# Kernel tuning notes

Hardware: AMD Instinct MI355X
Metric: run time of the kernel (lower is better)

## Reference

```python
import jax, jax.numpy as jnp
import numpy as np

B, N, D = 32, 2048, 1024


def setup_inputs() -> dict:
    key = jax.random.key(0)
    k1, k2, k3, k4, k5, k6 = jax.random.split(key, 6)
    encoded = jax.random.normal(k1, (B, N, D), dtype=jnp.float32)
    decoder_state = jax.random.normal(k2, (B, D), dtype=jnp.float32)
    mask = jax.random.randint(k3, (B, N), 0, 2, dtype=jnp.int32)
    scale = 1.0 / np.sqrt(D)
    W1 = jax.random.normal(k4, (D, D), dtype=jnp.float32) * scale  # applied as x @ W1
    W2 = jax.random.normal(k5, (D, D), dtype=jnp.float32) * scale
    vt = jax.random.normal(k6, (D,), dtype=jnp.float32) * scale
    return {"encoded": encoded, "decoder_state": decoder_state, "mask": mask,
            "W1": W1, "W2": W2, "vt": vt}


def reference(encoded, decoder_state, mask, W1, W2, vt):
    temperature = 1.0
    # process_encoded: W1(encoded)  [B, N, D]
    enc = jnp.einsum('bnd,de->bne', encoded, W1)
    # W2(decoder_state)  [B, D] -> broadcast-add over N
    dec = decoder_state @ W2
    # vt(tanh(.)).squeeze(2)  -> logits [B, N]
    u = jnp.einsum('bnd,d->bn', jnp.tanh(enc + dec[:, None, :]), vt)
    # masked log-softmax with temperature over dim=1
    logits = u / temperature + jnp.log(mask.astype(u.dtype) + 1e-45)
    return jax.nn.log_softmax(logits, axis=1)
```

## Files before the change

### kernel.cpp

```cpp
#include <hip/hip_runtime.h>

typedef _Float16 half8 __attribute__((ext_vector_type(8)));
typedef __fp16   pk2   __attribute__((ext_vector_type(2)));
typedef float    f32x4 __attribute__((ext_vector_type(4)));

#define GLOBAL_AS __attribute__((address_space(1)))
#define LDS_AS    __attribute__((address_space(3)))

static constexpr int Bb = 32;
static constexpr int Nn = 2048;
static constexpr int Dd = 1024;
static constexpr int M  = Bb * Nn;

__global__ void prep_w1(const float* __restrict__ W1, _Float16* __restrict__ W1TT) {
    int g = blockIdx.x * 256 + threadIdx.x;
    int tile = g >> 9;
    int u = g & 511;
    int et = tile >> 5, kt = tile & 31;
    int q = u >> 7, e = u & 127;
    int d0 = kt * 32 + q * 8;
    int col = et * 128 + e;
    half8 h;
#pragma unroll
    for (int j = 0; j < 8; ++j)
        h[j] = (_Float16)W1[(size_t)(d0 + j) * Dd + col];
    *(half8*)(W1TT + (size_t)g * 8) = h;
}

__global__ void prep_enc(const float* __restrict__ A, _Float16* __restrict__ A_p) {
    int g = blockIdx.x * 256 + threadIdx.x;
    int tile = g >> 9;
    int v = g & 511;
    int row = v >> 2, kc = v & 3;
    const float* src = A + ((size_t)(tile >> 5) * 128 + row) * Dd
                         + (tile & 31) * 32 + kc * 8;
    f32x4 f0 = *(const f32x4*)src;
    f32x4 f1 = *(const f32x4*)(src + 4);
    half8 h;
    pk2 t;
    t = __builtin_amdgcn_cvt_pkrtz(f0.x, f0.y); h[0] = t[0]; h[1] = t[1];
    t = __builtin_amdgcn_cvt_pkrtz(f0.z, f0.w); h[2] = t[0]; h[3] = t[1];
    t = __builtin_amdgcn_cvt_pkrtz(f1.x, f1.y); h[4] = t[0]; h[5] = t[1];
    t = __builtin_amdgcn_cvt_pkrtz(f1.z, f1.w); h[6] = t[0]; h[7] = t[1];
    *(half8*)(A_p + (size_t)g * 8) = h;
}

__global__ void dec_kernel(const float* __restrict__ ds, const float* __restrict__ W2,
                           float* __restrict__ dec) {
    __shared__ float part[4][64];
    int b = blockIdx.x, ech = blockIdx.y;
    int tid = threadIdx.x;
    int e = ech * 64 + (tid & 63);
    int dc = tid >> 6;
    float acc = 0.f;
#pragma unroll 4
    for (int d = dc * 256; d < dc * 256 + 256; ++d)
        acc += ds[b * Dd + d] * W2[(size_t)d * Dd + e];
    part[dc][tid & 63] = acc;
    __syncthreads();
    if (tid < 64)
        dec[b * Dd + e] = part[0][tid] + part[1][tid] + part[2][tid] + part[3][tid];
}

__global__ __launch_bounds__(256) void gemm_fused_h(
    const _Float16* __restrict__ A_p,
    const _Float16* __restrict__ W1TT,
    const float* __restrict__ dec,
    const float* __restrict__ vt,
    float* __restrict__ u_part)
{
    __shared__ _Float16 As[4096];
    __shared__ _Float16 Bs[4096];
    __shared__ float usum[2][128];

    const int g = blockIdx.x;
    const int et = (g >> 3) & 7;
    const int mtile = (g & 7) + ((g >> 6) << 3);
    const int tid = threadIdx.x;
    const int lane = tid & 63, wid = tid >> 6;
    const int wm = wid & 1, we = wid >> 1;
    const int q = lane >> 4, l15 = lane & 15;

    f32x4 acc[4][4] = {};

    const _Float16* abase = A_p + (size_t)mtile * 32 * 4096
                            + ((size_t)(wid * 2) * 64 + lane) * 8;
    const _Float16* bbase = W1TT + (size_t)et * 32 * 4096
                            + ((size_t)(wid * 2) * 64 + lane) * 8;
    _Float16* adst0 = &As[(wid * 2 + 0) * 64 * 8];
    _Float16* adst1 = &As[(wid * 2 + 1) * 64 * 8];
    _Float16* bdst0 = &Bs[(wid * 2 + 0) * 64 * 8];
    _Float16* bdst1 = &Bs[(wid * 2 + 1) * 64 * 8];

#pragma unroll 1
    for (int kt = 0; kt < 32; ++kt) {
        const _Float16* ak = abase + (size_t)kt * 4096;
        const _Float16* bk = bbase + (size_t)kt * 4096;
        __builtin_amdgcn_global_load_lds((const GLOBAL_AS void*)ak,
                                         (LDS_AS void*)adst0, 16, 0, 0);
        __builtin_amdgcn_global_load_lds((const GLOBAL_AS void*)(ak + 64 * 8),
                                         (LDS_AS void*)adst1, 16, 0, 0);
        __builtin_amdgcn_global_load_lds((const GLOBAL_AS void*)bk,
                                         (LDS_AS void*)bdst0, 16, 0, 0);
        __builtin_amdgcn_global_load_lds((const GLOBAL_AS void*)(bk + 64 * 8),
                                         (LDS_AS void*)bdst1, 16, 0, 0);
        __syncthreads();

        half8 af[4], bf[4];
#pragma unroll
        for (int mt = 0; mt < 4; ++mt)
            af[mt] = *(const half8*)&As[(wm * 64 + mt * 16 + l15) * 32 + q * 8];
#pragma unroll
        for (int nt = 0; nt < 4; ++nt)
            bf[nt] = *(const half8*)&Bs[(q * 128 + we * 64 + nt * 16 + l15) * 8];
#pragma unroll
        for (int mt = 0; mt < 4; ++mt)
#pragma unroll
            for (int nt = 0; nt < 4; ++nt)
                acc[mt][nt] = __builtin_amdgcn_mfma_f32_16x16x32_f16(
                    af[mt], bf[nt], acc[mt][nt], 0, 0, 0);
        __syncthreads();
    }

    const int b = mtile >> 4;
    float vtv[4], dcv[4];
#pragma unroll
    for (int nt = 0; nt < 4; ++nt) {
        int e = et * 128 + we * 64 + nt * 16 + l15;
        vtv[nt] = vt[e];
        dcv[nt] = dec[b * Dd + e];
    }
#pragma unroll
    for (int mt = 0; mt < 4; ++mt) {
#pragma unroll
        for (int r = 0; r < 4; ++r) {
            float s = 0.f;
#pragma unroll
            for (int nt = 0; nt < 4; ++nt) {
                float x = acc[mt][nt][r] + dcv[nt];
                float ex = __expf(2.f * x);
                float th = 1.f - 2.f * __builtin_amdgcn_rcpf(ex + 1.f);
                s += th * vtv[nt];
            }
#pragma unroll
            for (int off = 1; off < 16; off <<= 1) s += __shfl_xor(s, off, 16);
            if (l15 == 0) usum[we][wm * 64 + mt * 16 + q * 4 + r] = s;
        }
    }
    __syncthreads();
    if (tid < 128)
        u_part[(size_t)et * M + (size_t)mtile * 128 + tid] = usum[0][tid] + usum[1][tid];
}

__global__ __launch_bounds__(256) void gemm_fused_f32(
    const float* __restrict__ A, const _Float16* __restrict__ W1TT,
    const float* __restrict__ dec, const float* __restrict__ vt,
    float* __restrict__ u_part)
{
    __shared__ _Float16 As2[4 * 128 * 8];
    __shared__ _Float16 Bs2[512 * 8];
    __shared__ float usum[2][128];

    const int et = blockIdx.x, mtile = blockIdx.y;
    const int tid = threadIdx.x;
    const int lane = tid & 63, wid = tid >> 6;
    const int wm = wid & 1, we = wid >> 1;
    const int q = lane >> 4, l15 = lane & 15;
    f32x4 acc[4][4] = {};

    const int arow = tid >> 1, khalf = tid & 1;
    const float* aptr = A + (size_t)(mtile * 128 + arow) * Dd + khalf * 16;
    const int q0 = khalf * 2;
    const _Float16* bbase = W1TT + (size_t)et * 32 * 4096
                            + ((size_t)(wid * 2) * 64 + lane) * 8;
    _Float16* bdst0 = &Bs2[(wid * 2 + 0) * 64 * 8];
    _Float16* bdst1 = &Bs2[(wid * 2 + 1) * 64 * 8];

#pragma unroll 1
    for (int kt = 0; kt < 32; ++kt) {
        const _Float16* bk = bbase + (size_t)kt * 4096;
        __builtin_amdgcn_global_load_lds((const GLOBAL_AS void*)bk,
                                         (LDS_AS void*)bdst0, 16, 0, 0);
        __builtin_amdgcn_global_load_lds((const GLOBAL_AS void*)(bk + 64 * 8),
                                         (LDS_AS void*)bdst1, 16, 0, 0);
        const float4* ap = (const float4*)(aptr + kt * 32);
        float4 f0 = ap[0], f1 = ap[1], f2 = ap[2], f3 = ap[3];
        half8 h0, h1;
        {
            pk2 t;
            t = __builtin_amdgcn_cvt_pkrtz(f0.x, f0.y); h0[0] = t[0]; h0[1] = t[1];
            t = __builtin_amdgcn_cvt_pkrtz(f0.z, f0.w); h0[2] = t[0]; h0[3] = t[1];
            t = __builtin_amdgcn_cvt_pkrtz(f1.x, f1.y); h0[4] = t[0]; h0[5] = t[1];
            t = __builtin_amdgcn_cvt_pkrtz(f1.z, f1.w); h0[6] = t[0]; h0[7] = t[1];
            t = __builtin_amdgcn_cvt_pkrtz(f2.x, f2.y); h1[0] = t[0]; h1[1] = t[1];
            t = __builtin_amdgcn_cvt_pkrtz(f2.z, f2.w); h1[2] = t[0]; h1[3] = t[1];
            t = __builtin_amdgcn_cvt_pkrtz(f3.x, f3.y); h1[4] = t[0]; h1[5] = t[1];
            t = __builtin_amdgcn_cvt_pkrtz(f3.z, f3.w); h1[6] = t[0]; h1[7] = t[1];
        }
        *(half8*)&As2[((q0 + 0) * 128 + arow) * 8] = h0;
        *(half8*)&As2[((q0 + 1) * 128 + arow) * 8] = h1;
        __syncthreads();

        half8 af[4], bf[4];
#pragma unroll
        for (int mt = 0; mt < 4; ++mt)
            af[mt] = *(const half8*)&As2[(q * 128 + wm * 64 + mt * 16 + l15) * 8];
#pragma unroll
        for (int nt = 0; nt < 4; ++nt)
            bf[nt] = *(const half8*)&Bs2[(q * 128 + we * 64 + nt * 16 + l15) * 8];
#pragma unroll
        for (int mt = 0; mt < 4; ++mt)
#pragma unroll
            for (int nt = 0; nt < 4; ++nt)
                acc[mt][nt] = __builtin_amdgcn_mfma_f32_16x16x32_f16(
                    af[mt], bf[nt], acc[mt][nt], 0, 0, 0);
        __syncthreads();
    }

    const int b = mtile >> 4;
    float vtv[4], dcv[4];
#pragma unroll
    for (int nt = 0; nt < 4; ++nt) {
        int e = et * 128 + we * 64 + nt * 16 + l15;
        vtv[nt] = vt[e];
        dcv[nt] = dec[b * Dd + e];
    }
#pragma unroll
    for (int mt = 0; mt < 4; ++mt) {
#pragma unroll
        for (int r = 0; r < 4; ++r) {
            float s = 0.f;
#pragma unroll
            for (int nt = 0; nt < 4; ++nt) {
                float x = acc[mt][nt][r] + dcv[nt];
                float ex = __expf(2.f * x);
                float th = 1.f - 2.f * __builtin_amdgcn_rcpf(ex + 1.f);
                s += th * vtv[nt];
            }
#pragma unroll
            for (int off = 1; off < 16; off <<= 1) s += __shfl_xor(s, off, 16);
            if (l15 == 0) usum[we][wm * 64 + mt * 16 + q * 4 + r] = s;
        }
    }
    __syncthreads();
    if (tid < 128)
        u_part[(size_t)et * M + (size_t)mtile * 128 + tid] = usum[0][tid] + usum[1][tid];
}

__global__ void softmax_k(const float* __restrict__ up, const int* __restrict__ mask,
                          float* __restrict__ out) {
    __shared__ float red[8];
    int b = blockIdx.x, tid = threadIdx.x;
    float l[8];
#pragma unroll
    for (int i = 0; i < 8; ++i) {
        int n = i * 256 + tid;
        float s = up[(size_t)b * Nn + n];
#pragma unroll
        for (int et = 1; et < 8; ++et) s += up[(size_t)et * M + (size_t)b * Nn + n];
        l[i] = s + (mask[b * Nn + n] ? 0.f : -103.278931f);
    }
    float m = l[0];
#pragma unroll
    for (int i = 1; i < 8; ++i) m = fmaxf(m, l[i]);
#pragma unroll
    for (int o = 32; o >= 1; o >>= 1) m = fmaxf(m, __shfl_xor(m, o, 64));
    if ((tid & 63) == 0) red[tid >> 6] = m;
    __syncthreads();
    m = fmaxf(fmaxf(red[0], red[1]), fmaxf(red[2], red[3]));
    float s = 0.f;
#pragma unroll
    for (int i = 0; i < 8; ++i) s += expf(l[i] - m);
#pragma unroll
    for (int o = 32; o >= 1; o >>= 1) s += __shfl_xor(s, o, 64);
    if ((tid & 63) == 0) red[4 + (tid >> 6)] = s;
    __syncthreads();
    float lse = m + logf(red[4] + red[5] + red[6] + red[7]);
#pragma unroll
    for (int i = 0; i < 8; ++i)
        out[(size_t)b * Nn + i * 256 + tid] = l[i] - lse;
}

extern "C" void kernel_launch(void* const* d_in, const int* in_sizes, int n_in,
                              void* d_out, int out_size, void* d_ws, size_t ws_size,
                              hipStream_t stream) {
    const float* encoded = (const float*)d_in[0];
    const float* dstate  = (const float*)d_in[1];
    const int*   mask    = (const int*)d_in[2];
    const float* W1      = (const float*)d_in[3];
    const float* W2      = (const float*)d_in[4];
    const float* vt      = (const float*)d_in[5];
    float* out = (float*)d_out;

    char* ws = (char*)d_ws;
    float*    u_part = (float*)ws;
    float*    dec    = (float*)(ws + (size_t)8 * M * 4);
    _Float16* W1TT   = (_Float16*)(ws + (size_t)8 * M * 4 + (size_t)Bb * Dd * 4);
    _Float16* A_p    = (_Float16*)(ws + (size_t)8 * M * 4 + (size_t)Bb * Dd * 4
                                   + (size_t)Dd * Dd * 2);
    const size_t needed = (size_t)8 * M * 4 + (size_t)Bb * Dd * 4
                        + (size_t)Dd * Dd * 2 + (size_t)M * Dd * 2;

    prep_w1<<<512, 256, 0, stream>>>(W1, W1TT);
    dec_kernel<<<dim3(32, 16), 256, 0, stream>>>(dstate, W2, dec);
    if (ws_size >= needed) {
        prep_enc<<<32768, 256, 0, stream>>>(encoded, A_p);
        gemm_fused_h<<<4096, 256, 0, stream>>>(A_p, W1TT, dec, vt, u_part);
    } else {
        gemm_fused_f32<<<dim3(8, 512), 256, 0, stream>>>(encoded, W1TT, dec, vt, u_part);
    }
    softmax_k<<<32, 256, 0, stream>>>(u_part, mask, out);
}
```

Baseline: 610.0 us.

## Double-buffer LDS tiles in fused GEMM to overlap loads with MFMA

The fused fp16 GEMM kernel now uses two LDS buffers for the A and B tiles. The next k-tile is prefetched with global_load_lds while the MFMAs for the current tile run, and synchronisation uses explicit s_waitcnt vmcnt and s_barrier. The vt and dec epilogue loads are hoisted before the main loop. This aims to hide global-memory latency, at the cost of doubled LDS use (lower occupancy) and relying on hand-written waitcnt counts being correct.

Result: faster. 593.0 us (-2.8%).

```diff
diff --git a/kernel.cpp b/kernel.cpp
--- a/kernel.cpp
+++ b/kernel.cpp
@@ -69,8 +69,8 @@
     const float* __restrict__ vt,
     float* __restrict__ u_part)
 {
-    __shared__ _Float16 As[4096];
-    __shared__ _Float16 Bs[4096];
+    __shared__ _Float16 As[2][4096];
+    __shared__ _Float16 Bs[2][4096];
     __shared__ float usum[2][128];
 
     const int g = blockIdx.x;
@@ -83,53 +83,68 @@
 
     f32x4 acc[4][4] = {};
 
+    const int b = mtile >> 4;
+    float vtv[4], dcv[4];
+#pragma unroll
+    for (int nt = 0; nt < 4; ++nt) {
+        int e = et * 128 + we * 64 + nt * 16 + l15;
+        vtv[nt] = vt[e];
+        dcv[nt] = dec[b * Dd + e];
+    }
+    asm volatile("s_waitcnt vmcnt(0)" ::: "memory");
+
     const _Float16* abase = A_p + (size_t)mtile * 32 * 4096
                             + ((size_t)(wid * 2) * 64 + lane) * 8;
     const _Float16* bbase = W1TT + (size_t)et * 32 * 4096
                             + ((size_t)(wid * 2) * 64 + lane) * 8;
-    _Float16* adst0 = &As[(wid * 2 + 0) * 64 * 8];
-    _Float16* adst1 = &As[(wid * 2 + 1) * 64 * 8];
-    _Float16* bdst0 = &Bs[(wid * 2 + 0) * 64 * 8];
-    _Float16* bdst1 = &Bs[(wid * 2 + 1) * 64 * 8];
+    _Float16* adst[2] = { &As[0][(wid * 2) * 64 * 8], &As[1][(wid * 2) * 64 * 8] };
+    _Float16* bdst[2] = { &Bs[0][(wid * 2) * 64 * 8], &Bs[1][(wid * 2) * 64 * 8] };
+
+    auto issue = [&](int kt) {
+        const _Float16* ak = abase + (size_t)kt * 4096;
+        const _Float16* bk = bbase + (size_t)kt * 4096;
+        const int s = kt & 1;
+        __builtin_amdgcn_global_load_lds((const GLOBAL_AS void*)ak,
+                                         (LDS_AS void*)adst[s], 16, 0, 0);
+        __builtin_amdgcn_global_load_lds((const GLOBAL_AS void*)(ak + 512),
+                                         (LDS_AS void*)(adst[s] + 512), 16, 0, 0);
+        __builtin_amdgcn_global_load_lds((const GLOBAL_AS void*)bk,
+                                         (LDS_AS void*)bdst[s], 16, 0, 0);
+        __builtin_amdgcn_global_load_lds((const GLOBAL_AS void*)(bk + 512),
+                                         (LDS_AS void*)(bdst[s] + 512), 16, 0, 0);
+    };
+
+    issue(0);
 
 #pragma unroll 1
     for (int kt = 0; kt < 32; ++kt) {
-        const _Float16* ak = abase + (size_t)kt * 4096;
-        const _Float16* bk = bbase + (size_t)kt * 4096;
-        __builtin_amdgcn_global_load_lds((const GLOBAL_AS void*)ak,
-                                         (LDS_AS void*)adst0, 16, 0, 0);
-        __builtin_amdgcn_global_load_lds((const GLOBAL_AS void*)(ak + 64 * 8),
-                                         (LDS_AS void*)adst1, 16, 0, 0);
-        __builtin_amdgcn_global_load_lds((const GLOBAL_AS void*)bk,
-                                         (LDS_AS void*)bdst0, 16, 0, 0);
-        __builtin_amdgcn_global_load_lds((const GLOBAL_AS void*)(bk + 64 * 8),
-                                         (LDS_AS void*)bdst1, 16, 0, 0);
-        __syncthreads();
+        const int s = kt & 1;
+        if (kt < 31) {
+            issue(kt + 1);
+            asm volatile("s_waitcnt vmcnt(4)" ::: "memory");
+        } else {
+            asm volatile("s_waitcnt vmcnt(0)" ::: "memory");
+        }
+        asm volatile("s_barrier" ::: "memory");
 
         half8 af[4], bf[4];
 #pragma unroll
         for (int mt = 0; mt < 4; ++mt)
-            af[mt] = *(const half8*)&As[(wm * 64 + mt * 16 + l15) * 32 + q * 8];
+            af[mt] = *(const half8*)&As[s][(wm * 64 + mt * 16 + l15) * 32 + q * 8];
 #pragma unroll
         for (int nt = 0; nt < 4; ++nt)
-            bf[nt] = *(const half8*)&Bs[(q * 128 + we * 64 + nt * 16 + l15) * 8];
+            bf[nt] = *(const half8*)&Bs[s][(q * 128 + we * 64 + nt * 16 + l15) * 8];
 #pragma unroll
         for (int mt = 0; mt < 4; ++mt)
 #pragma unroll
             for (int nt = 0; nt < 4; ++nt)
                 acc[mt][nt] = __builtin_amdgcn_mfma_f32_16x16x32_f16(
                     af[mt], bf[nt], acc[mt][nt], 0, 0, 0);
-        __syncthreads();
-    }
-
-    const int b = mtile >> 4;
-    float vtv[4], dcv[4];
-#pragma unroll
-    for (int nt = 0; nt < 4; ++nt) {
-        int e = et * 128 + we * 64 + nt * 16 + l15;
-        vtv[nt] = vt[e];
-        dcv[nt] = dec[b * Dd + e];
-    }
+
+        asm volatile("s_waitcnt lgkmcnt(0)" ::: "memory");
+        asm volatile("s_barrier" ::: "memory");
+    }
+
 #pragma unroll
     for (int mt = 0; mt < 4; ++mt) {
 #pragma unroll
@@ -181,7 +196,7 @@
         const _Float16* bk = bbase + (size_t)kt * 4096;
         __builtin_amdgcn_global_load_lds((const GLOBAL_AS void*)bk,
                                          (LDS_AS void*)bdst0, 16, 0, 0);
-        __builtin_amdgcn_global_load_lds((const GLOBAL_AS void*)(bk + 64 * 8),
+        __builtin_amdgcn_global_load_lds((const GLOBAL_AS void*)(bk + 512),
                                          (LDS_AS void*)bdst1, 16, 0, 0);
         const float4* ap = (const float4*)(aptr + kt * 32);
         float4 f0 = ap[0], f1 = ap[1], f2 = ap[2], f3 = ap[3];
```
